# Performance work log

Measured on AMD Instinct MI355X. Metric: run time of the kernel, lower is better.

Reference implementation:

```python
import jax, jax.numpy as jnp
import numpy as np

B, T, IN, H, OUT = 64, 512, 512, 1024, 1


def _uniform(key, shape, stdv):
    return jax.random.uniform(key, shape, jnp.float32, -stdv, stdv)


def setup_inputs() -> dict:
    key = jax.random.key(0)
    ks = jax.random.split(key, 12)
    stdv = 1.0 / H ** 0.5
    x = jax.random.normal(ks[0], (B, T, IN), jnp.float32)
    # layer 0 cell (input_size=IN), layer 1 cell (input_size=H)
    w_ih0 = _uniform(ks[1], (4 * H, IN), stdv)
    w_hh0 = _uniform(ks[2], (4 * H, H), stdv)
    b_ih0 = _uniform(ks[3], (4 * H,), stdv)
    b_hh0 = _uniform(ks[4], (4 * H,), stdv)
    w_ih1 = _uniform(ks[5], (4 * H, H), stdv)
    w_hh1 = _uniform(ks[6], (4 * H, H), stdv)
    b_ih1 = _uniform(ks[7], (4 * H,), stdv)
    b_hh1 = _uniform(ks[8], (4 * H,), stdv)
    # nn.Linear default init: U(-1/sqrt(fan_in), 1/sqrt(fan_in))
    s_out = 1.0 / H ** 0.5
    w_out = _uniform(ks[9], (OUT, H), s_out)
    b_out = _uniform(ks[10], (OUT,), s_out)
    return dict(x=x, w_ih0=w_ih0, w_hh0=w_hh0, b_ih0=b_ih0, b_hh0=b_hh0,
                w_ih1=w_ih1, w_hh1=w_hh1, b_ih1=b_ih1, b_hh1=b_hh1,
                w_out=w_out, b_out=b_out)


def _lstm_layer(x_tbi, w_ih, w_hh, b_ih, b_hh):
    # x_tbi: [T, B, in]. Batch the input-to-hidden GEMM over all timesteps.
    gx = jnp.einsum('tbi,gi->tbg', x_tbi, w_ih) + b_ih + b_hh  # [T,B,4H]

    def step(carry, gxt):
        h, c = carry
        gates = gxt + h @ w_hh.T  # [B,4H]
        i, f, g, o = jnp.split(gates, 4, axis=1)
        c = jax.nn.sigmoid(f) * c + jax.nn.sigmoid(i) * jnp.tanh(g)
        h = jax.nn.sigmoid(o) * jnp.tanh(c)
        return (h, c), h

    h0 = jnp.zeros((x_tbi.shape[1], w_hh.shape[1]), x_tbi.dtype)
    (_, _), hs = jax.lax.scan(step, (h0, h0), gx)
    return hs  # [T,B,H]


def reference(x, w_ih0, w_hh0, b_ih0, b_hh0, w_ih1, w_hh1, b_ih1, b_hh1, w_out, b_out):
    xt = jnp.transpose(x, (1, 0, 2))  # [T,B,IN] (batch_first)
    h1 = _lstm_layer(xt, w_ih0, w_hh0, b_ih0, b_hh0)
    h2 = _lstm_layer(h1, w_ih1, w_hh1, b_ih1, b_hh1)
    out = jnp.einsum('tbh,oh->tbo', h2, w_out) + b_out  # [T,B,OUT]
    return jnp.transpose(out, (1, 0, 2))  # [B,T,OUT]
```

## Files before the change

### kernel.cpp

```cpp
#include <hip/hip_runtime.h>

#define T_SEQ 512
#define B_SZ  64
#define IN_SZ 512
#define H_SZ  1024
#define NBLK  256
#define NTHR  512

#define FLG_STRIDE 4
#define FLG_ROW    (128 * FLG_STRIDE)

typedef _Float16 f16;
typedef _Float16 half8 __attribute__((ext_vector_type(8)));
typedef float    f32x4 __attribute__((ext_vector_type(4)));

#define SM_WFRAG 0
#define SM_PART  131072
#define SM_C     (131072 + 8192)
#define SM_BIAS  (131072 + 8192 + 2048)
#define SM_STAGE (131072 + 8192 + 2048 + 128)
#define SMEM_BYTES (131072 + 8192 + 2048 + 128 + 1024)

struct Params {
    const float *x;
    const float *wih0, *whh0, *bih0, *bhh0;
    const float *wih1, *whh1, *bih1, *bhh1;
    f16 *h1all;
    f16 *h2all;
    int *flg0, *flg1;
};

__device__ __forceinline__ float sigf(float x)     { return 1.f / (1.f + __expf(-x)); }
__device__ __forceinline__ float tanhfast(float x) { return 2.f / (1.f + __expf(-2.f * x)) - 1.f; }

__global__ __launch_bounds__(NTHR, 2) void persist_kernel(Params p)
{
    extern __shared__ char smem[];
    f16*   wfrag = (f16*)(smem + SM_WFRAG);
    float* P     = (float*)(smem + SM_PART);
    float* c_lds = (float*)(smem + SM_C);
    float* bl    = (float*)(smem + SM_BIAS);
    f16*   hst   = (f16*)(smem + SM_STAGE);

    const int tid = threadIdx.x;
    const int l   = tid & 63, wv = tid >> 6;
    const int n16 = l & 15,  q  = l >> 4;
    const int mt  = wv & 3,  kp = wv >> 2;
    const int layer = blockIdx.x >> 7;
    const int bid   = blockIdx.x & 127;
    const int jb    = bid * 8;

    {
        const int gate0 = n16 >> 3, c8 = n16 & 7;
        const int nfrag = layer ? 128 : 96;
        for (int f = wv; f < nfrag; f += 8) {
            int kstep = f >> 1, nt = f & 1;
            int wrow = (nt * 2 + gate0) * H_SZ + jb + c8;
            const float* src;
            if (layer == 0) {
                src = (kstep < 16) ? p.wih0 + (size_t)wrow * IN_SZ + kstep * 32 + q * 8
                                   : p.whh0 + (size_t)wrow * H_SZ + (kstep - 16) * 32 + q * 8;
            } else {
                src = (kstep < 32) ? p.wih1 + (size_t)wrow * H_SZ + kstep * 32 + q * 8
                                   : p.whh1 + (size_t)wrow * H_SZ + (kstep - 32) * 32 + q * 8;
            }
            half8 hv;
            #pragma unroll
            for (int u = 0; u < 8; ++u) hv[u] = (f16)src[u];
            *(half8*)(wfrag + f * 512 + l * 8) = hv;
        }
        if (tid < 32) {
            int gate = tid >> 3, col = tid & 7;
            int wrow = gate * H_SZ + jb + col;
            bl[tid] = layer ? (p.bih1[wrow] + p.bhh1[wrow])
                            : (p.bih0[wrow] + p.bhh0[wrow]);
        }
        c_lds[tid] = 0.f;
    }
    __syncthreads();

    auto ldB = [&](int kg, int nt) -> half8 {
        return *(const half8*)(wfrag + (kg * 2 + nt) * 512 + l * 8);
    };
    auto wtile = [&](int slot, const f32x4& v) {
        *(f32x4*)(P + slot * 256 + l * 4) = v;
    };
    auto atile = [&](int slot, f32x4& a) {
        a += *(const f32x4*)(P + slot * 256 + l * 4);
    };
    int* myflg = layer ? p.flg1 : p.flg0;

    for (int s = 0; s < T_SEQ; ++s) {
        f32x4 acc0 = {}, acc1 = {};

        if (layer == 0) {
            #pragma unroll
            for (int u = 0; u < 8; ++u) {
                int kg = kp * 8 + u;
                int kb = kg * 32 + q * 8;
                half8 b0 = ldB(kg, 0), b1 = ldB(kg, 1);
                const float* ap = p.x + ((size_t)(mt * 16 + n16) * T_SEQ + s) * IN_SZ + kb;
                f32x4 xa = *(const f32x4*)ap;
                f32x4 xb = *(const f32x4*)(ap + 4);
                half8 af;
                #pragma unroll
                for (int u2 = 0; u2 < 4; ++u2) { af[u2] = (f16)xa[u2]; af[4 + u2] = (f16)xb[u2]; }
                acc0 = __builtin_amdgcn_mfma_f32_16x16x32_f16(af, b0, acc0, 0, 0, 0);
                acc1 = __builtin_amdgcn_mfma_f32_16x16x32_f16(af, b1, acc1, 0, 0, 0);
            }
            if (s > 0) {
                if (wv == 0) {
                    const int* f = p.flg0 + (size_t)(s - 1) * FLG_ROW;
                    const int* a0 = f + l * FLG_STRIDE;
                    const int* a1 = f + (l + 64) * FLG_STRIDE;
                    while (true) {
                        int va = __hip_atomic_load(a0, __ATOMIC_RELAXED, __HIP_MEMORY_SCOPE_AGENT);
                        int vb = __hip_atomic_load(a1, __ATOMIC_RELAXED, __HIP_MEMORY_SCOPE_AGENT);
                        if (__all(va & vb)) break;
                        __builtin_amdgcn_s_sleep(1);
                    }
                }
                __syncthreads();
                const f16* hp = p.h1all + (size_t)(s - 1) * (B_SZ * H_SZ);
                #pragma unroll
                for (int u = 0; u < 16; ++u) {
                    int kg = 16 + kp * 16 + u;
                    int kb = (kg - 16) * 32 + q * 8;
                    half8 b0 = ldB(kg, 0), b1 = ldB(kg, 1);
                    half8 af = *(const half8*)(hp + (size_t)(mt * 16 + n16) * H_SZ + kb);
                    acc0 = __builtin_amdgcn_mfma_f32_16x16x32_f16(af, b0, acc0, 0, 0, 0);
                    acc1 = __builtin_amdgcn_mfma_f32_16x16x32_f16(af, b1, acc1, 0, 0, 0);
                }
            }
        } else {
            {
                if (wv == 0) {
                    const int* fA = p.flg0 + (size_t)s * FLG_ROW;
                    const int* a0 = fA + l * FLG_STRIDE;
                    const int* a1 = fA + (l + 64) * FLG_STRIDE;
                    if (s == 0) {
                        while (true) {
                            int va = __hip_atomic_load(a0, __ATOMIC_RELAXED, __HIP_MEMORY_SCOPE_AGENT);
                            int vb = __hip_atomic_load(a1, __ATOMIC_RELAXED, __HIP_MEMORY_SCOPE_AGENT);
                            if (__all(va & vb)) break;
                            __builtin_amdgcn_s_sleep(1);
                        }
                    } else {
                        const int* fB = p.flg1 + (size_t)(s - 1) * FLG_ROW;
                        const int* b0 = fB + l * FLG_STRIDE;
                        const int* b1 = fB + (l + 64) * FLG_STRIDE;
                        while (true) {
                            int va = __hip_atomic_load(a0, __ATOMIC_RELAXED, __HIP_MEMORY_SCOPE_AGENT);
                            int vb = __hip_atomic_load(a1, __ATOMIC_RELAXED, __HIP_MEMORY_SCOPE_AGENT);
                            int vc = __hip_atomic_load(b0, __ATOMIC_RELAXED, __HIP_MEMORY_SCOPE_AGENT);
                            int vd = __hip_atomic_load(b1, __ATOMIC_RELAXED, __HIP_MEMORY_SCOPE_AGENT);
                            if (__all(va & vb & vc & vd)) break;
                            __builtin_amdgcn_s_sleep(1);
                        }
                    }
                }
                __syncthreads();
            }
            {
                const f16* hp = p.h1all + (size_t)s * (B_SZ * H_SZ);
                #pragma unroll
                for (int u = 0; u < 16; ++u) {
                    int kg = kp * 16 + u;
                    int kb = kg * 32 + q * 8;
                    half8 b0 = ldB(kg, 0), b1 = ldB(kg, 1);
                    half8 af = *(const half8*)(hp + (size_t)(mt * 16 + n16) * H_SZ + kb);
                    acc0 = __builtin_amdgcn_mfma_f32_16x16x32_f16(af, b0, acc0, 0, 0, 0);
                    acc1 = __builtin_amdgcn_mfma_f32_16x16x32_f16(af, b1, acc1, 0, 0, 0);
                }
            }
            if (s > 0) {
                const f16* hp = p.h2all + (size_t)(s - 1) * (B_SZ * H_SZ);
                #pragma unroll
                for (int u = 0; u < 16; ++u) {
                    int kg = 32 + kp * 16 + u;
                    int kb = (kg - 32) * 32 + q * 8;
                    half8 b0 = ldB(kg, 0), b1 = ldB(kg, 1);
                    half8 af = *(const half8*)(hp + (size_t)(mt * 16 + n16) * H_SZ + kb);
                    acc0 = __builtin_amdgcn_mfma_f32_16x16x32_f16(af, b0, acc0, 0, 0, 0);
                    acc1 = __builtin_amdgcn_mfma_f32_16x16x32_f16(af, b1, acc1, 0, 0, 0);
                }
            }
        }

        if (kp == 1) {
            wtile(mt * 2 + 0, acc0);
            wtile(mt * 2 + 1, acc1);
        }
        __syncthreads();
        if (kp == 0) {
            atile(mt * 2 + 0, acc0);
            atile(mt * 2 + 1, acc1);
            wtile(mt * 2 + 0, acc0);
            wtile(mt * 2 + 1, acc1);
        }
        __syncthreads();

        {
            int b = tid >> 3, col = tid & 7;
            int bmt = b >> 4, r = b & 15;
            int base = (r >> 2) * 64 + (r & 3);
            float iv = P[(bmt * 2 + 0) * 256 + base + col * 4]       + bl[col];
            float fv = P[(bmt * 2 + 0) * 256 + base + (col + 8) * 4] + bl[8 + col];
            float gv = P[(bmt * 2 + 1) * 256 + base + col * 4]       + bl[16 + col];
            float ov = P[(bmt * 2 + 1) * 256 + base + (col + 8) * 4] + bl[24 + col];
            float co = c_lds[tid];
            float ii = sigf(iv), ff = sigf(fv), gg = tanhfast(gv), oo = sigf(ov);
            float cn = ff * co + ii * gg;
            float hn = oo * tanhfast(cn);
            c_lds[tid] = cn;
            hst[b * 8 + col] = (f16)hn;
        }
        __syncthreads();
        if (tid < 128) {
            int b = tid >> 1, half = tid & 1;
            unsigned long long v = *(const unsigned long long*)(hst + b * 8 + half * 4);
            f16* dst = (layer ? p.h2all : p.h1all) + (size_t)s * (B_SZ * H_SZ);
            __hip_atomic_store((unsigned long long*)(dst + (size_t)b * H_SZ + jb + half * 4), v,
                               __ATOMIC_RELAXED, __HIP_MEMORY_SCOPE_AGENT);
        }
        __syncthreads();
        if (tid == 0)
            __hip_atomic_store(myflg + (size_t)s * FLG_ROW + bid * FLG_STRIDE, 1,
                               __ATOMIC_RELAXED, __HIP_MEMORY_SCOPE_AGENT);
    }
}

__global__ __launch_bounds__(256) void gemv_kernel(
    const f16* __restrict__ h2all, const float* __restrict__ wout,
    const float* __restrict__ bout, float* __restrict__ out)
{
    int t = blockIdx.x;
    int wave = threadIdx.x >> 6, lane = threadIdx.x & 63;
    float w[16];
    #pragma unroll
    for (int u = 0; u < 16; ++u) w[u] = wout[lane * 16 + u];
    float b0 = bout[0];
    for (int b = wave; b < B_SZ; b += 4) {
        const f16* hp = h2all + ((size_t)t * B_SZ + b) * H_SZ + lane * 16;
        float sum = 0.f;
        #pragma unroll
        for (int u = 0; u < 16; ++u) sum += (float)hp[u] * w[u];
        #pragma unroll
        for (int off = 32; off; off >>= 1) sum += __shfl_down(sum, off, 64);
        if (lane == 0) out[(size_t)b * T_SEQ + t] = sum + b0;
    }
}

extern "C" void kernel_launch(void* const* d_in, const int* in_sizes, int n_in,
                              void* d_out, int out_size, void* d_ws, size_t ws_size,
                              hipStream_t stream)
{
    const float* x    = (const float*)d_in[0];
    const float* wih0 = (const float*)d_in[1];
    const float* whh0 = (const float*)d_in[2];
    const float* bih0 = (const float*)d_in[3];
    const float* bhh0 = (const float*)d_in[4];
    const float* wih1 = (const float*)d_in[5];
    const float* whh1 = (const float*)d_in[6];
    const float* bih1 = (const float*)d_in[7];
    const float* bhh1 = (const float*)d_in[8];
    const float* wout = (const float*)d_in[9];
    const float* bout = (const float*)d_in[10];
    float* out = (float*)d_out;

    char* ws = (char*)d_ws;
    size_t off = 0;
    auto alloc = [&](size_t bytes) -> void* {
        void* pp = ws + off;
        off += (bytes + 255) & ~(size_t)255;
        return pp;
    };
    f16* h1all = (f16*)alloc((size_t)T_SEQ * B_SZ * H_SZ * 2);
    f16* h2all = (f16*)alloc((size_t)T_SEQ * B_SZ * H_SZ * 2);
    const size_t flg_bytes = (size_t)2 * T_SEQ * FLG_ROW * 4;
    int* flgs  = (int*)alloc(flg_bytes);

    (void)hipMemsetAsync(flgs, 0, flg_bytes, stream);

    Params pa;
    pa.x = x;
    pa.wih0 = wih0; pa.whh0 = whh0; pa.bih0 = bih0; pa.bhh0 = bhh0;
    pa.wih1 = wih1; pa.whh1 = whh1; pa.bih1 = bih1; pa.bhh1 = bhh1;
    pa.h1all = h1all; pa.h2all = h2all;
    pa.flg0 = flgs; pa.flg1 = flgs + T_SEQ * FLG_ROW;

    (void)hipFuncSetAttribute((const void*)persist_kernel,
                              hipFuncAttributeMaxDynamicSharedMemorySize, SMEM_BYTES);

    hipStreamCaptureStatus cap = hipStreamCaptureStatusNone;
    (void)hipStreamIsCapturing(stream, &cap);
    bool launched = false;
    if (cap == hipStreamCaptureStatusNone) {
        void* kargs[] = { (void*)&pa };
        if (hipLaunchCooperativeKernel((const void*)persist_kernel, dim3(NBLK), dim3(NTHR),
                                       kargs, SMEM_BYTES, stream) == hipSuccess)
            launched = true;
    }
    if (!launched)
        persist_kernel<<<NBLK, NTHR, SMEM_BYTES, stream>>>(pa);

    gemv_kernel<<<T_SEQ, 256, 0, stream>>>(h2all, wout, bout, out);
}
```

Baseline: 5.607 ms.

## Hoist weight fragments into registers, reorder layer-1 recurrence, drop partial-sum reduction barrier

Preloads most weight fragments from LDS into registers once, before the time loop, so each step no longer reloads them. Layer 1 now runs its own-recurrence GEMM (h2 from the previous step) before waiting on layer 0's flag, so that work overlaps with layer 0's progress. Split-K partials are written to separate LDS slots and summed in the gate computation, which removes one barrier and a read-modify-write pass. The cost is heavy register pressure under launch_bounds(512,2), which may cause spills, plus a larger LDS footprint.

Result: faster. 4.973 ms (-11.3%).

```diff
diff --git a/kernel.cpp b/kernel.cpp
--- a/kernel.cpp
+++ b/kernel.cpp
@@ -16,10 +16,10 @@
 
 #define SM_WFRAG 0
 #define SM_PART  131072
-#define SM_C     (131072 + 8192)
-#define SM_BIAS  (131072 + 8192 + 2048)
-#define SM_STAGE (131072 + 8192 + 2048 + 128)
-#define SMEM_BYTES (131072 + 8192 + 2048 + 128 + 1024)
+#define SM_C     (131072 + 16384)
+#define SM_BIAS  (131072 + 16384 + 2048)
+#define SM_STAGE (131072 + 16384 + 2048 + 128)
+#define SMEM_BYTES (131072 + 16384 + 2048 + 128 + 1024)
 
 struct Params {
     const float *x;
@@ -82,132 +82,32 @@
     auto ldB = [&](int kg, int nt) -> half8 {
         return *(const half8*)(wfrag + (kg * 2 + nt) * 512 + l * 8);
     };
-    auto wtile = [&](int slot, const f32x4& v) {
-        *(f32x4*)(P + slot * 256 + l * 4) = v;
-    };
-    auto atile = [&](int slot, f32x4& a) {
-        a += *(const f32x4*)(P + slot * 256 + l * 4);
-    };
-    int* myflg = layer ? p.flg1 : p.flg0;
-
-    for (int s = 0; s < T_SEQ; ++s) {
-        f32x4 acc0 = {}, acc1 = {};
-
-        if (layer == 0) {
-            #pragma unroll
-            for (int u = 0; u < 8; ++u) {
-                int kg = kp * 8 + u;
-                int kb = kg * 32 + q * 8;
-                half8 b0 = ldB(kg, 0), b1 = ldB(kg, 1);
-                const float* ap = p.x + ((size_t)(mt * 16 + n16) * T_SEQ + s) * IN_SZ + kb;
-                f32x4 xa = *(const f32x4*)ap;
-                f32x4 xb = *(const f32x4*)(ap + 4);
-                half8 af;
-                #pragma unroll
-                for (int u2 = 0; u2 < 4; ++u2) { af[u2] = (f16)xa[u2]; af[4 + u2] = (f16)xb[u2]; }
-                acc0 = __builtin_amdgcn_mfma_f32_16x16x32_f16(af, b0, acc0, 0, 0, 0);
-                acc1 = __builtin_amdgcn_mfma_f32_16x16x32_f16(af, b1, acc1, 0, 0, 0);
-            }
-            if (s > 0) {
-                if (wv == 0) {
-                    const int* f = p.flg0 + (size_t)(s - 1) * FLG_ROW;
-                    const int* a0 = f + l * FLG_STRIDE;
-                    const int* a1 = f + (l + 64) * FLG_STRIDE;
-                    while (true) {
-                        int va = __hip_atomic_load(a0, __ATOMIC_RELAXED, __HIP_MEMORY_SCOPE_AGENT);
-                        int vb = __hip_atomic_load(a1, __ATOMIC_RELAXED, __HIP_MEMORY_SCOPE_AGENT);
-                        if (__all(va & vb)) break;
-                        __builtin_amdgcn_s_sleep(1);
-                    }
-                }
-                __syncthreads();
-                const f16* hp = p.h1all + (size_t)(s - 1) * (B_SZ * H_SZ);
-                #pragma unroll
-                for (int u = 0; u < 16; ++u) {
-                    int kg = 16 + kp * 16 + u;
-                    int kb = (kg - 16) * 32 + q * 8;
-                    half8 b0 = ldB(kg, 0), b1 = ldB(kg, 1);
-                    half8 af = *(const half8*)(hp + (size_t)(mt * 16 + n16) * H_SZ + kb);
-                    acc0 = __builtin_amdgcn_mfma_f32_16x16x32_f16(af, b0, acc0, 0, 0, 0);
-                    acc1 = __builtin_amdgcn_mfma_f32_16x16x32_f16(af, b1, acc1, 0, 0, 0);
-                }
-            }
-        } else {
-            {
-                if (wv == 0) {
-                    const int* fA = p.flg0 + (size_t)s * FLG_ROW;
-                    const int* a0 = fA + l * FLG_STRIDE;
-                    const int* a1 = fA + (l + 64) * FLG_STRIDE;
-                    if (s == 0) {
-                        while (true) {
-                            int va = __hip_atomic_load(a0, __ATOMIC_RELAXED, __HIP_MEMORY_SCOPE_AGENT);
-                            int vb = __hip_atomic_load(a1, __ATOMIC_RELAXED, __HIP_MEMORY_SCOPE_AGENT);
-                            if (__all(va & vb)) break;
-                            __builtin_amdgcn_s_sleep(1);
-                        }
-                    } else {
-                        const int* fB = p.flg1 + (size_t)(s - 1) * FLG_ROW;
-                        const int* b0 = fB + l * FLG_STRIDE;
-                        const int* b1 = fB + (l + 64) * FLG_STRIDE;
-                        while (true) {
-                            int va = __hip_atomic_load(a0, __ATOMIC_RELAXED, __HIP_MEMORY_SCOPE_AGENT);
-                            int vb = __hip_atomic_load(a1, __ATOMIC_RELAXED, __HIP_MEMORY_SCOPE_AGENT);
-                            int vc = __hip_atomic_load(b0, __ATOMIC_RELAXED, __HIP_MEMORY_SCOPE_AGENT);
-                            int vd = __hip_atomic_load(b1, __ATOMIC_RELAXED, __HIP_MEMORY_SCOPE_AGENT);
-                            if (__all(va & vb & vc & vd)) break;
-                            __builtin_amdgcn_s_sleep(1);
-                        }
-                    }
-                }
-                __syncthreads();
-            }
-            {
-                const f16* hp = p.h1all + (size_t)s * (B_SZ * H_SZ);
-                #pragma unroll
-                for (int u = 0; u < 16; ++u) {
-                    int kg = kp * 16 + u;
-                    int kb = kg * 32 + q * 8;
-                    half8 b0 = ldB(kg, 0), b1 = ldB(kg, 1);
-                    half8 af = *(const half8*)(hp + (size_t)(mt * 16 + n16) * H_SZ + kb);
-                    acc0 = __builtin_amdgcn_mfma_f32_16x16x32_f16(af, b0, acc0, 0, 0, 0);
-                    acc1 = __builtin_amdgcn_mfma_f32_16x16x32_f16(af, b1, acc1, 0, 0, 0);
-                }
-            }
-            if (s > 0) {
-                const f16* hp = p.h2all + (size_t)(s - 1) * (B_SZ * H_SZ);
-                #pragma unroll
-                for (int u = 0; u < 16; ++u) {
-                    int kg = 32 + kp * 16 + u;
-                    int kb = (kg - 32) * 32 + q * 8;
-                    half8 b0 = ldB(kg, 0), b1 = ldB(kg, 1);
-                    half8 af = *(const half8*)(hp + (size_t)(mt * 16 + n16) * H_SZ + kb);
-                    acc0 = __builtin_amdgcn_mfma_f32_16x16x32_f16(af, b0, acc0, 0, 0, 0);
-                    acc1 = __builtin_amdgcn_mfma_f32_16x16x32_f16(af, b1, acc1, 0, 0, 0);
-                }
-            }
-        }
-
-        if (kp == 1) {
-            wtile(mt * 2 + 0, acc0);
-            wtile(mt * 2 + 1, acc1);
-        }
+    auto pollAll = [&](const int* fl) {
+        const int* a0 = fl + l * FLG_STRIDE;
+        const int* a1 = fl + (l + 64) * FLG_STRIDE;
+        while (true) {
+            int va = __hip_atomic_load(a0, __ATOMIC_RELAXED, __HIP_MEMORY_SCOPE_AGENT);
+            int vb = __hip_atomic_load(a1, __ATOMIC_RELAXED, __HIP_MEMORY_SCOPE_AGENT);
+            if (__all(va & vb)) break;
+            __builtin_amdgcn_s_sleep(1);
+        }
+    };
+    auto finish = [&](int s, const f32x4& acc0, const f32x4& acc1,
+                      f16* dstAll, int* myflg) {
+        int slot = kp * 8 + mt * 2;
+        *(f32x4*)(P + (slot + 0) * 256 + l * 4) = acc0;
+        *(f32x4*)(P + (slot + 1) * 256 + l * 4) = acc1;
         __syncthreads();
-        if (kp == 0) {
-            atile(mt * 2 + 0, acc0);
-            atile(mt * 2 + 1, acc1);
-            wtile(mt * 2 + 0, acc0);
-            wtile(mt * 2 + 1, acc1);
-        }
-        __syncthreads();
-
         {
             int b = tid >> 3, col = tid & 7;
             int bmt = b >> 4, r = b & 15;
             int base = (r >> 2) * 64 + (r & 3);
-            float iv = P[(bmt * 2 + 0) * 256 + base + col * 4]       + bl[col];
-            float fv = P[(bmt * 2 + 0) * 256 + base + (col + 8) * 4] + bl[8 + col];
-            float gv = P[(bmt * 2 + 1) * 256 + base + col * 4]       + bl[16 + col];
-            float ov = P[(bmt * 2 + 1) * 256 + base + (col + 8) * 4] + bl[24 + col];
+            int s0 = (bmt * 2 + 0) * 256 + base;
+            int s1 = (bmt * 2 + 1) * 256 + base;
+            float iv = P[s0 + col * 4]        + P[s0 + 2048 + col * 4]        + bl[col];
+            float fv = P[s0 + (col + 8) * 4]  + P[s0 + 2048 + (col + 8) * 4]  + bl[8 + col];
+            float gv = P[s1 + col * 4]        + P[s1 + 2048 + col * 4]        + bl[16 + col];
+            float ov = P[s1 + (col + 8) * 4]  + P[s1 + 2048 + (col + 8) * 4]  + bl[24 + col];
             float co = c_lds[tid];
             float ii = sigf(iv), ff = sigf(fv), gg = tanhfast(gv), oo = sigf(ov);
             float cn = ff * co + ii * gg;
@@ -219,7 +119,7 @@
         if (tid < 128) {
             int b = tid >> 1, half = tid & 1;
             unsigned long long v = *(const unsigned long long*)(hst + b * 8 + half * 4);
-            f16* dst = (layer ? p.h2all : p.h1all) + (size_t)s * (B_SZ * H_SZ);
+            f16* dst = dstAll + (size_t)s * (B_SZ * H_SZ);
             __hip_atomic_store((unsigned long long*)(dst + (size_t)b * H_SZ + jb + half * 4), v,
                                __ATOMIC_RELAXED, __HIP_MEMORY_SCOPE_AGENT);
         }
@@ -227,6 +127,86 @@
         if (tid == 0)
             __hip_atomic_store(myflg + (size_t)s * FLG_ROW + bid * FLG_STRIDE, 1,
                                __ATOMIC_RELAXED, __HIP_MEMORY_SCOPE_AGENT);
+    };
+
+    if (layer == 0) {
+        half8 brx0[8], brx1[8], brr0[16], brr1[16];
+        #pragma unroll
+        for (int u = 0; u < 8; ++u)  { int kg = kp * 8 + u;       brx0[u] = ldB(kg, 0); brx1[u] = ldB(kg, 1); }
+        #pragma unroll
+        for (int u = 0; u < 16; ++u) { int kg = 16 + kp * 16 + u; brr0[u] = ldB(kg, 0); brr1[u] = ldB(kg, 1); }
+
+        for (int s = 0; s < T_SEQ; ++s) {
+            f32x4 acc0 = {}, acc1 = {};
+            #pragma unroll
+            for (int u = 0; u < 8; ++u) {
+                int kb = (kp * 8 + u) * 32 + q * 8;
+                const float* ap = p.x + ((size_t)(mt * 16 + n16) * T_SEQ + s) * IN_SZ + kb;
+                f32x4 xa = *(const f32x4*)ap;
+                f32x4 xb = *(const f32x4*)(ap + 4);
+                half8 af;
+                #pragma unroll
+                for (int u2 = 0; u2 < 4; ++u2) { af[u2] = (f16)xa[u2]; af[4 + u2] = (f16)xb[u2]; }
+                acc0 = __builtin_amdgcn_mfma_f32_16x16x32_f16(af, brx0[u], acc0, 0, 0, 0);
+                acc1 = __builtin_amdgcn_mfma_f32_16x16x32_f16(af, brx1[u], acc1, 0, 0, 0);
+            }
+            if (s > 0) {
+                if (wv == 0) pollAll(p.flg0 + (size_t)(s - 1) * FLG_ROW);
+                __syncthreads();
+                const f16* hp = p.h1all + (size_t)(s - 1) * (B_SZ * H_SZ)
+                              + (size_t)(mt * 16 + n16) * H_SZ + kp * 512 + q * 8;
+                #pragma unroll
+                for (int u = 0; u < 16; ++u) {
+                    half8 af = *(const half8*)(hp + u * 32);
+                    acc0 = __builtin_amdgcn_mfma_f32_16x16x32_f16(af, brr0[u], acc0, 0, 0, 0);
+                    acc1 = __builtin_amdgcn_mfma_f32_16x16x32_f16(af, brr1[u], acc1, 0, 0, 0);
+                }
+            }
+            finish(s, acc0, acc1, p.h1all, p.flg0);
+        }
+    } else {
+        half8 bri0[16], bri1[16], brr0[8], brr1[8];
+        #pragma unroll
+        for (int u = 0; u < 16; ++u) { int kg = kp * 16 + u;      bri0[u] = ldB(kg, 0); bri1[u] = ldB(kg, 1); }
+        #pragma unroll
+        for (int u = 0; u < 8; ++u)  { int kg = 32 + kp * 16 + u; brr0[u] = ldB(kg, 0); brr1[u] = ldB(kg, 1); }
+
+        for (int s = 0; s < T_SEQ; ++s) {
+            f32x4 acc0 = {}, acc1 = {};
+            if (s > 0) {
+                if (wv == 0) pollAll(p.flg1 + (size_t)(s - 1) * FLG_ROW);
+                __syncthreads();
+                const f16* hp = p.h2all + (size_t)(s - 1) * (B_SZ * H_SZ)
+                              + (size_t)(mt * 16 + n16) * H_SZ + kp * 512 + q * 8;
+                #pragma unroll
+                for (int u = 0; u < 8; ++u) {
+                    half8 af = *(const half8*)(hp + u * 32);
+                    acc0 = __builtin_amdgcn_mfma_f32_16x16x32_f16(af, brr0[u], acc0, 0, 0, 0);
+                    acc1 = __builtin_amdgcn_mfma_f32_16x16x32_f16(af, brr1[u], acc1, 0, 0, 0);
+                }
+                #pragma unroll
+                for (int u = 8; u < 16; ++u) {
+                    int kg = 32 + kp * 16 + u;
+                    half8 b0 = ldB(kg, 0), b1 = ldB(kg, 1);
+                    half8 af = *(const half8*)(hp + u * 32);
+                    acc0 = __builtin_amdgcn_mfma_f32_16x16x32_f16(af, b0, acc0, 0, 0, 0);
+                    acc1 = __builtin_amdgcn_mfma_f32_16x16x32_f16(af, b1, acc1, 0, 0, 0);
+                }
+            }
+            if (wv == 0) pollAll(p.flg0 + (size_t)s * FLG_ROW);
+            __syncthreads();
+            {
+                const f16* hp = p.h1all + (size_t)s * (B_SZ * H_SZ)
+                              + (size_t)(mt * 16 + n16) * H_SZ + kp * 512 + q * 8;
+                #pragma unroll
+                for (int u = 0; u < 16; ++u) {
+                    half8 af = *(const half8*)(hp + u * 32);
+                    acc0 = __builtin_amdgcn_mfma_f32_16x16x32_f16(af, bri0[u], acc0, 0, 0, 0);
+                    acc1 = __builtin_amdgcn_mfma_f32_16x16x32_f16(af, bri1[u], acc1, 0, 0, 0);
+                }
+            }
+            finish(s, acc0, acc1, p.h2all, p.flg1);
+        }
     }
 }
 
```
